# Optimization experiments

Hardware: AMD Instinct MI355X
Metric: run time of the kernel (lower is better)

The kernel has to match this reference:

```python
import jax, jax.numpy as jnp
import numpy as np

NEG_SLOPE = 0.2


def setup_inputs() -> dict:
    key = jax.random.key(0)
    k1, k2, k3 = jax.random.split(key, 3)
    bs, n_agents, input_dim = 32, 512, 128
    n_heads, hidden_dim = 8, 64
    h = jax.random.normal(k1, (bs, n_agents, input_dim), dtype=jnp.float32)
    # Linear(input_dim, n_heads*hidden_dim, bias=False), stored as [in, out]
    W = jax.random.normal(k2, (input_dim, n_heads * hidden_dim), dtype=jnp.float32) * (1.0 / np.sqrt(input_dim))
    # xavier_uniform with gain=1.414 on shape (1, n_heads, 2*hidden_dim)
    fan = n_heads + 2 * hidden_dim
    bound = 1.414 * np.sqrt(6.0 / fan)
    att_a = jax.random.uniform(k3, (1, n_heads, 2 * hidden_dim), dtype=jnp.float32,
                               minval=-bound, maxval=bound)
    return {"h": h, "W": W, "att_a": att_a}


def reference(h, W, att_a):
    bs, n_agents, _ = h.shape
    n_heads = att_a.shape[1]
    hidden_dim = att_a.shape[2] // 2
    # h_prime: [bs, n_heads, n_agents, hidden_dim]
    h_prime = (h @ W).reshape(bs, n_agents, n_heads, hidden_dim).transpose(0, 2, 1, 3)
    # Additive score decomposes exactly: (a1.h_i + a2.h_j) == sum(cat(h_i,h_j)*a)
    a_src = att_a[0, :, :hidden_dim]   # [n_heads, hidden_dim]
    a_dst = att_a[0, :, hidden_dim:]   # [n_heads, hidden_dim]
    e_src = jnp.einsum('bhnd,hd->bhn', h_prime, a_src)  # score contribution of node i (row)
    e_dst = jnp.einsum('bhnd,hd->bhn', h_prime, a_dst)  # contribution of node j (col)
    e = e_src[:, :, :, None] + e_dst[:, :, None, :]     # [bs, n_heads, n, n]
    e = jnp.where(e >= 0, e, NEG_SLOPE * e)             # leaky_relu(0.2)
    attention = jax.nn.softmax(e, axis=-1)
    h_new = jnp.einsum('bhnm,bhmd->bhnd', attention, h_prime)
    return jax.nn.elu(h_new)
```

## Files before the change

### kernel.cpp

```cpp
#include <hip/hip_runtime.h>

#define BS 32
#define NA 512
#define ID 128
#define NH 8
#define HD 64
#define NHD 512
#define NEG 0.2f
#define NC 32
#define CH 16
#define NW 8
#define BPAD 136

typedef short bf16x8 __attribute__((ext_vector_type(8)));
typedef float f32x4 __attribute__((ext_vector_type(4)));

__device__ inline unsigned f2bf_bits(float x) {
  unsigned u = __float_as_uint(x);
  return (u + 0x7FFFu + ((u >> 16) & 1u)) >> 16;
}

__device__ inline void split8(const float4& x, const float4& y,
                              bf16x8& hi, bf16x8& lo) {
  float f[8] = {x.x, x.y, x.z, x.w, y.x, y.y, y.z, y.w};
  #pragma unroll
  for (int j = 0; j < 8; ++j) {
    unsigned hb = f2bf_bits(f[j]);
    float r = f[j] - __uint_as_float(hb << 16);
    unsigned lb = f2bf_bits(r);
    hi[j] = (short)hb;
    lo[j] = (short)lb;
  }
}

__global__ __launch_bounds__(256, 4) void k1_mfma(
    const float* __restrict__ h, const float* __restrict__ W,
    float* __restrict__ io) {
  __shared__ unsigned short Bhi[64 * BPAD];
  __shared__ unsigned short Blo[64 * BPAD];

  int blk = blockIdx.x;
  int mt = blk >> 3;
  int n0 = (blk & 7) * 64;
  int m0 = mt * 128;
  int b = mt >> 2;
  int nbase = (mt & 3) * 128;
  int head = n0 >> 6;
  int t = threadIdx.x;
  int lane = t & 63, w = t >> 6;
  int q = lane >> 4, ml = lane & 15;

  {
    int c = t & 63, kq = t >> 6;
    const float* wsrc = W + (size_t)kq * 32 * NHD + n0 + c;
    #pragma unroll 4
    for (int kk = 0; kk < 32; ++kk) {
      int k = kq * 32 + kk;
      float x = wsrc[(size_t)kk * NHD];
      unsigned hb = f2bf_bits(x);
      float r = x - __uint_as_float(hb << 16);
      Bhi[c * BPAD + k] = (unsigned short)hb;
      Blo[c * BPAD + k] = (unsigned short)f2bf_bits(r);
    }
  }
  __syncthreads();

  f32x4 acc[2][4];
  #pragma unroll
  for (int mf = 0; mf < 2; ++mf)
    #pragma unroll
    for (int nf = 0; nf < 4; ++nf)
      acc[mf][nf] = (f32x4){0.f, 0.f, 0.f, 0.f};

  const float* A0 = h + (size_t)(m0 + w * 32 + ml) * ID;

  #pragma unroll
  for (int ks = 0; ks < 4; ++ks) {
    int ko = ks * 32 + q * 8;
    bf16x8 ah[2], al[2];
    #pragma unroll
    for (int mf = 0; mf < 2; ++mf) {
      const float* ap = A0 + mf * 16 * ID + ko;
      float4 f0 = *(const float4*)ap;
      float4 f1 = *(const float4*)(ap + 4);
      split8(f0, f1, ah[mf], al[mf]);
    }
    #pragma unroll
    for (int nf = 0; nf < 4; ++nf) {
      int bo = (nf * 16 + ml) * BPAD + ko;
      bf16x8 bh = *(const bf16x8*)&Bhi[bo];
      bf16x8 bl = *(const bf16x8*)&Blo[bo];
      #pragma unroll
      for (int mf = 0; mf < 2; ++mf) {
        acc[mf][nf] = __builtin_amdgcn_mfma_f32_16x16x32_bf16(ah[mf], bh, acc[mf][nf], 0, 0, 0);
        acc[mf][nf] = __builtin_amdgcn_mfma_f32_16x16x32_bf16(ah[mf], bl, acc[mf][nf], 0, 0, 0);
        acc[mf][nf] = __builtin_amdgcn_mfma_f32_16x16x32_bf16(al[mf], bh, acc[mf][nf], 0, 0, 0);
      }
    }
  }

  {
    float* ob = io + (((size_t)b * NH + head) * NA + nbase + w * 32) * HD + ml;
    #pragma unroll
    for (int mf = 0; mf < 2; ++mf)
      #pragma unroll
      for (int nf = 0; nf < 4; ++nf)
        #pragma unroll
        for (int r = 0; r < 4; ++r)
          ob[(size_t)(mf * 16 + q * 4 + r) * HD + nf * 16] = acc[mf][nf][r];
  }
}

__global__ __launch_bounds__(512, 2) void k2_fused(
    const float* __restrict__ att, float* __restrict__ io) {
  __shared__ float tv[NA]; __shared__ int tpm[NA];
  __shared__ float sv[NA]; __shared__ int spm[NA];
  __shared__ float wp[NA]; __shared__ float wn[NA];
  __shared__ float rawP8[NW * 64]; __shared__ float rawN8[NW * 64];
  __shared__ float sufPc[(NW + 1) * 64]; __shared__ float preNc[(NW + 1) * 64];
  __shared__ float zps[NA + 1]; __shared__ float znp[NA + 1];
  __shared__ float szP[NC]; __shared__ float szN[NC];
  __shared__ float sufZ[NC + 1]; __shared__ float preZ[NC + 1];
  __shared__ float4 abi[NA];
  __shared__ int jsr[NA];
  __shared__ int Earr[NA];
  __shared__ float asrc[HD]; __shared__ float adst[HD];

  int bh = blockIdx.x;
  int head = bh & (NH - 1);
  int t = threadIdx.x;
  int lane = t & 63, w = t >> 6;
  float* vbase = io + (size_t)bh * NA * HD;

  if (t < 2 * HD) {
    float a = att[head * 2 * HD + t];
    if (t < HD) asrc[t] = a; else adst[t - HD] = a;
  }
  __syncthreads();

  float vt, vs; int it = t, is_ = t;
  {
    const float4* vr = (const float4*)(vbase + (size_t)t * HD);
    float s0 = 0.f, s1 = 0.f, t0 = 0.f, t1 = 0.f;
    #pragma unroll
    for (int j = 0; j < HD / 4; j += 2) {
      float4 v0 = vr[j], v1 = vr[j + 1];
      s0 += v0.x*asrc[4*j+0] + v0.y*asrc[4*j+1] + v0.z*asrc[4*j+2] + v0.w*asrc[4*j+3];
      t0 += v0.x*adst[4*j+0] + v0.y*adst[4*j+1] + v0.z*adst[4*j+2] + v0.w*adst[4*j+3];
      s1 += v1.x*asrc[4*j+4] + v1.y*asrc[4*j+5] + v1.z*asrc[4*j+6] + v1.w*asrc[4*j+7];
      t1 += v1.x*adst[4*j+4] + v1.y*adst[4*j+5] + v1.z*adst[4*j+6] + v1.w*adst[4*j+7];
    }
    vs = s0 + s1; vt = t0 + t1;
  }

  for (int size = 2; size <= NA; size <<= 1) {
    bool dirAsc = ((t & size) == 0);
    for (int stride = size >> 1; stride > 0; stride >>= 1) {
      float pt, ps; int pit, pis;
      if (stride >= 64) {
        tv[t] = vt; tpm[t] = it; sv[t] = vs; spm[t] = is_;
        __syncthreads();
        pt = tv[t ^ stride]; pit = tpm[t ^ stride];
        ps = sv[t ^ stride]; pis = spm[t ^ stride];
        __syncthreads();
      } else {
        pt = __shfl_xor(vt, stride, 64); pit = __shfl_xor(it, stride, 64);
        ps = __shfl_xor(vs, stride, 64); pis = __shfl_xor(is_, stride, 64);
      }
      bool mn = (((t & stride) == 0) == dirAsc);
      if (mn ? (pt < vt) : (pt > vt)) { vt = pt; it = pit; }
      if (mn ? (ps < vs) : (ps > vs)) { vs = ps; is_ = pis; }
    }
  }
  tv[t] = vt; tpm[t] = it; sv[t] = vs; spm[t] = is_;
  __syncthreads();

  float cmax = fmaxf(tv[NA - 1], 0.f);
  float amax = fmaxf(sv[NA - 1], 0.f);
  wp[t] = __expf(vt - cmax);
  wn[t] = __expf(NEG * vt - cmax);
  __syncthreads();

  float vreg[64];
  {
    float aP = 0.f, aN = 0.f;
    #pragma unroll
    for (int jj = 0; jj < 64; ++jj) {
      int j = (w << 6) + jj;
      float vv = vbase[(size_t)tpm[j] * HD + lane];
      vreg[jj] = vv;
      aP += wp[j] * vv;
      aN += wn[j] * vv;
    }
    rawP8[(w << 6) + lane] = aP;
    rawN8[(w << 6) + lane] = aN;
  }
  __syncthreads();

  if (t < 64) {
    int d = t; float run = 0.f;
    sufPc[NW * 64 + d] = 0.f;
    for (int ww = NW - 1; ww >= 0; --ww) {
      run += rawP8[ww * 64 + d]; sufPc[ww * 64 + d] = run;
    }
  } else if (t < 128) {
    int d = t - 64; float run = 0.f;
    for (int ww = 0; ww <= NW; ++ww) {
      preNc[ww * 64 + d] = run;
      if (ww < NW) run += rawN8[ww * 64 + d];
    }
  } else if (t < 160) {
    int c = t - 128; float a = 0.f;
    for (int j = c * CH; j < c * CH + CH; ++j) a += wp[j];
    szP[c] = a;
  } else if (t < 192) {
    int c = t - 160; float a = 0.f;
    for (int j = c * CH; j < c * CH + CH; ++j) a += wn[j];
    szN[c] = a;
  }
  __syncthreads();

  if (t == 0) {
    float run = 0.f; sufZ[NC] = 0.f;
    for (int cc = NC - 1; cc >= 0; --cc) { run += szP[cc]; sufZ[cc] = run; }
  } else if (t == 1) {
    float run = 0.f;
    for (int cc = 0; cc <= NC; ++cc) { preZ[cc] = run; if (cc < NC) run += szN[cc]; }
  }
  __syncthreads();

  {
    int ch = t >> 4;
    float a = 0.f;
    for (int k = t; k < ch * CH + CH; ++k) a += wp[k];
    zps[t] = a + sufZ[ch + 1];
    float b2 = 0.f;
    for (int k = ch * CH; k < t; ++k) b2 += wn[k];
    znp[t] = preZ[ch] + b2;
    if (t == 0) { zps[NA] = 0.f; znp[NA] = preZ[NC]; }
  }
  __syncthreads();

  {
    float A = __expf(vs - amax);
    float B = __expf(NEG * vs - amax);
    float key = -vs;
    int lo = 0, hi = NA;
    while (lo < hi) { int mid = (lo + hi) >> 1; if (tv[mid] < key) lo = mid + 1; else hi = mid; }
    float den = A * zps[lo] + B * znp[lo];
    float4 qv; qv.x = A; qv.y = B; qv.z = 1.f / den; qv.w = __int_as_float(is_);
    abi[t] = qv;
    jsr[t] = lo;
  }
  __syncthreads();

  {
    int lo = 0, hi = NA;
    while (lo < hi) { int mid = (lo + hi) >> 1; if (jsr[mid] > t) lo = mid + 1; else hi = mid; }
    Earr[t] = lo;
  }
  __syncthreads();

  {
    float sufPv = sufPc[w * 64 + lane];
    float preSeedN = preNc[w * 64 + lane];
    float runN = 0.f;
    size_t obase = (size_t)bh * NA * HD + lane;
    int eprev = (w == 0) ? NA : Earr[(w << 6) - 1];
    #pragma unroll
    for (int jj = 0; jj < 64; ++jj) {
      int j = (w << 6) + jj;
      int ecur = Earr[j];
      float preNv = preSeedN + runN;
      for (int r = ecur; r < eprev; ++r) {
        float4 qv = abi[r];
        float x = (qv.x * sufPv + qv.y * preNv) * qv.z;
        int orow = __float_as_int(qv.w);
        io[obase + (size_t)orow * HD] = x > 0.f ? x : __expf(x) - 1.f;
      }
      float vv = vreg[jj];
      sufPv -= wp[j] * vv;
      runN  += wn[j] * vv;
      eprev = ecur;
    }
    if (w == NW - 1) {
      float preNv = preSeedN + runN;
      for (int r = 0; r < eprev; ++r) {
        float4 qv = abi[r];
        float x = (qv.y * preNv) * qv.z;
        int orow = __float_as_int(qv.w);
        io[obase + (size_t)orow * HD] = x > 0.f ? x : __expf(x) - 1.f;
      }
    }
  }
}

extern "C" void kernel_launch(void* const* d_in, const int* in_sizes, int n_in,
                              void* d_out, int out_size, void* d_ws, size_t ws_size,
                              hipStream_t stream) {
  const float* h   = (const float*)d_in[0];
  const float* W   = (const float*)d_in[1];
  const float* att = (const float*)d_in[2];
  float* io = (float*)d_out;
  (void)d_ws; (void)ws_size;

  k1_mfma <<<dim3(1024),    dim3(256), 0, stream>>>(h, W, io);
  k2_fused<<<dim3(BS * NH), dim3(512), 0, stream>>>(att, io);
}
```

Measured before the change: 126.1 us.

## Double attention-kernel block to 1024 threads and recompute per-row softmax factors inline

The fused attention kernel now runs with 1024 threads, or 16 waves, per block. Each wave sweeps 32 sorted columns instead of 64, and the sort and prefix-sum stages are guarded to the first 512 threads. The precomputed float4 per-row table (A, B, 1/den, row index) is removed. The output loop now recomputes the two exponentials and the reciprocal from the sorted scores and zps/znp, which saves shared memory and one barrier phase. This gives each CU more waves to hide global-store latency, at the cost of extra transcendental work per output element and idle threads in the sort phase.

After: 133.1 us. +5.5%, slower.

```diff
diff --git a/kernel.cpp b/kernel.cpp
--- a/kernel.cpp
+++ b/kernel.cpp
@@ -9,7 +9,7 @@
 #define NEG 0.2f
 #define NC 32
 #define CH 16
-#define NW 8
+#define NW2 16
 #define BPAD 136
 
 typedef short bf16x8 __attribute__((ext_vector_type(8)));
@@ -111,17 +111,15 @@
   }
 }
 
-__global__ __launch_bounds__(512, 2) void k2_fused(
+__global__ __launch_bounds__(1024) void k2_fused(
     const float* __restrict__ att, float* __restrict__ io) {
   __shared__ float tv[NA]; __shared__ int tpm[NA];
   __shared__ float sv[NA]; __shared__ int spm[NA];
   __shared__ float wp[NA]; __shared__ float wn[NA];
-  __shared__ float rawP8[NW * 64]; __shared__ float rawN8[NW * 64];
-  __shared__ float sufPc[(NW + 1) * 64]; __shared__ float preNc[(NW + 1) * 64];
+  __shared__ float sufPc[(NW2 + 1) * 64]; __shared__ float preNc[(NW2 + 1) * 64];
   __shared__ float zps[NA + 1]; __shared__ float znp[NA + 1];
   __shared__ float szP[NC]; __shared__ float szN[NC];
   __shared__ float sufZ[NC + 1]; __shared__ float preZ[NC + 1];
-  __shared__ float4 abi[NA];
   __shared__ int jsr[NA];
   __shared__ int Earr[NA];
   __shared__ float asrc[HD]; __shared__ float adst[HD];
@@ -138,8 +136,8 @@
   }
   __syncthreads();
 
-  float vt, vs; int it = t, is_ = t;
-  {
+  float vt = 0.f, vs = 0.f; int it = t, is_ = t;
+  if (t < NA) {
     const float4* vr = (const float4*)(vbase + (size_t)t * HD);
     float s0 = 0.f, s1 = 0.f, t0 = 0.f, t1 = 0.f;
     #pragma unroll
@@ -156,59 +154,72 @@
   for (int size = 2; size <= NA; size <<= 1) {
     bool dirAsc = ((t & size) == 0);
     for (int stride = size >> 1; stride > 0; stride >>= 1) {
-      float pt, ps; int pit, pis;
       if (stride >= 64) {
-        tv[t] = vt; tpm[t] = it; sv[t] = vs; spm[t] = is_;
+        if (t < NA) {
+          tv[t] = vt; tpm[t] = it; sv[t] = vs; spm[t] = is_;
+        }
         __syncthreads();
-        pt = tv[t ^ stride]; pit = tpm[t ^ stride];
-        ps = sv[t ^ stride]; pis = spm[t ^ stride];
+        if (t < NA) {
+          float pt = tv[t ^ stride]; int pit = tpm[t ^ stride];
+          float ps = sv[t ^ stride]; int pis = spm[t ^ stride];
+          bool mn = (((t & stride) == 0) == dirAsc);
+          if (mn ? (pt < vt) : (pt > vt)) { vt = pt; it = pit; }
+          if (mn ? (ps < vs) : (ps > vs)) { vs = ps; is_ = pis; }
+        }
         __syncthreads();
-      } else {
-        pt = __shfl_xor(vt, stride, 64); pit = __shfl_xor(it, stride, 64);
-        ps = __shfl_xor(vs, stride, 64); pis = __shfl_xor(is_, stride, 64);
+      } else if (t < NA) {
+        float pt = __shfl_xor(vt, stride, 64); int pit = __shfl_xor(it, stride, 64);
+        float ps = __shfl_xor(vs, stride, 64); int pis = __shfl_xor(is_, stride, 64);
+        bool mn = (((t & stride) == 0) == dirAsc);
+        if (mn ? (pt < vt) : (pt > vt)) { vt = pt; it = pit; }
+        if (mn ? (ps < vs) : (ps > vs)) { vs = ps; is_ = pis; }
       }
-      bool mn = (((t & stride) == 0) == dirAsc);
-      if (mn ? (pt < vt) : (pt > vt)) { vt = pt; it = pit; }
-      if (mn ? (ps < vs) : (ps > vs)) { vs = ps; is_ = pis; }
-    }
-  }
-  tv[t] = vt; tpm[t] = it; sv[t] = vs; spm[t] = is_;
+    }
+  }
+  if (t < NA) {
+    tv[t] = vt; tpm[t] = it; sv[t] = vs; spm[t] = is_;
+  }
   __syncthreads();
 
   float cmax = fmaxf(tv[NA - 1], 0.f);
   float amax = fmaxf(sv[NA - 1], 0.f);
-  wp[t] = __expf(vt - cmax);
-  wn[t] = __expf(NEG * vt - cmax);
-  __syncthreads();
-
-  float vreg[64];
+  if (t < NA) {
+    wp[t] = __expf(vt - cmax);
+    wn[t] = __expf(NEG * vt - cmax);
+  }
+  __syncthreads();
+
+  float vreg[32];
   {
     float aP = 0.f, aN = 0.f;
     #pragma unroll
-    for (int jj = 0; jj < 64; ++jj) {
-      int j = (w << 6) + jj;
+    for (int jj = 0; jj < 32; ++jj) {
+      int j = (w << 5) + jj;
       float vv = vbase[(size_t)tpm[j] * HD + lane];
       vreg[jj] = vv;
       aP += wp[j] * vv;
       aN += wn[j] * vv;
     }
-    rawP8[(w << 6) + lane] = aP;
-    rawN8[(w << 6) + lane] = aN;
+    sufPc[w * 64 + lane] = aP;
+    preNc[w * 64 + lane] = aN;
   }
   __syncthreads();
 
   if (t < 64) {
-    int d = t; float run = 0.f;
-    sufPc[NW * 64 + d] = 0.f;
-    for (int ww = NW - 1; ww >= 0; --ww) {
-      run += rawP8[ww * 64 + d]; sufPc[ww * 64 + d] = run;
+    float run = 0.f;
+    sufPc[NW2 * 64 + t] = 0.f;
+    for (int ww = NW2 - 1; ww >= 0; --ww) {
+      run += sufPc[ww * 64 + t];
+      sufPc[ww * 64 + t] = run;
     }
   } else if (t < 128) {
     int d = t - 64; float run = 0.f;
-    for (int ww = 0; ww <= NW; ++ww) {
+    for (int ww = 0; ww < NW2; ++ww) {
+      float raw = preNc[ww * 64 + d];
       preNc[ww * 64 + d] = run;
-      if (ww < NW) run += rawN8[ww * 64 + d];
-    }
+      run += raw;
+    }
+    preNc[NW2 * 64 + d] = run;
   } else if (t < 160) {
     int c = t - 128; float a = 0.f;
     for (int j = c * CH; j < c * CH + CH; ++j) a += wp[j];
@@ -229,7 +240,7 @@
   }
   __syncthreads();
 
-  {
+  if (t < NA) {
     int ch = t >> 4;
     float a = 0.f;
     for (int k = t; k < ch * CH + CH; ++k) a += wp[k];
@@ -238,23 +249,14 @@
     for (int k = ch * CH; k < t; ++k) b2 += wn[k];
     znp[t] = preZ[ch] + b2;
     if (t == 0) { zps[NA] = 0.f; znp[NA] = preZ[NC]; }
-  }
-  __syncthreads();
-
-  {
-    float A = __expf(vs - amax);
-    float B = __expf(NEG * vs - amax);
     float key = -vs;
     int lo = 0, hi = NA;
     while (lo < hi) { int mid = (lo + hi) >> 1; if (tv[mid] < key) lo = mid + 1; else hi = mid; }
-    float den = A * zps[lo] + B * znp[lo];
-    float4 qv; qv.x = A; qv.y = B; qv.z = 1.f / den; qv.w = __int_as_float(is_);
-    abi[t] = qv;
     jsr[t] = lo;
   }
   __syncthreads();
 
-  {
+  if (t < NA) {
     int lo = 0, hi = NA;
     while (lo < hi) { int mid = (lo + hi) >> 1; if (jsr[mid] > t) lo = mid + 1; else hi = mid; }
     Earr[t] = lo;
@@ -266,16 +268,19 @@
     float preSeedN = preNc[w * 64 + lane];
     float runN = 0.f;
     size_t obase = (size_t)bh * NA * HD + lane;
-    int eprev = (w == 0) ? NA : Earr[(w << 6) - 1];
-    #pragma unroll
-    for (int jj = 0; jj < 64; ++jj) {
-      int j = (w << 6) + jj;
+    int eprev = (w == 0) ? NA : Earr[(w << 5) - 1];
+    #pragma unroll 1
+    for (int jj = 0; jj < 32; ++jj) {
+      int j = (w << 5) + jj;
       int ecur = Earr[j];
       float preNv = preSeedN + runN;
       for (int r = ecur; r < eprev; ++r) {
-        float4 qv = abi[r];
-        float x = (qv.x * sufPv + qv.y * preNv) * qv.z;
-        int orow = __float_as_int(qv.w);
+        float s = sv[r];
+        float A = __expf(s - amax);
+        float B = __expf(NEG * s - amax);
+        float inv = 1.f / (A * zps[j] + B * znp[j]);
+        float x = (A * sufPv + B * preNv) * inv;
+        int orow = spm[r];
         io[obase + (size_t)orow * HD] = x > 0.f ? x : __expf(x) - 1.f;
       }
       float vv = vreg[jj];
@@ -283,12 +288,15 @@
       runN  += wn[j] * vv;
       eprev = ecur;
     }
-    if (w == NW - 1) {
+    if (w == NW2 - 1) {
       float preNv = preSeedN + runN;
       for (int r = 0; r < eprev; ++r) {
-        float4 qv = abi[r];
-        float x = (qv.y * preNv) * qv.z;
-        int orow = __float_as_int(qv.w);
+        float s = sv[r];
+        float A = __expf(s - amax);
+        float B = __expf(NEG * s - amax);
+        float inv = 1.f / (A * zps[NA] + B * znp[NA]);
+        float x = (B * preNv) * inv;
+        int orow = spm[r];
         io[obase + (size_t)orow * HD] = x > 0.f ? x : __expf(x) - 1.f;
       }
     }
@@ -304,6 +312,6 @@
   float* io = (float*)d_out;
   (void)d_ws; (void)ws_size;
 
-  k1_mfma <<<dim3(1024),    dim3(256), 0, stream>>>(h, W, io);
-  k2_fused<<<dim3(BS * NH), dim3(512), 0, stream>>>(att, io);
-}
+  k1_mfma <<<dim3(1024),    dim3(256),  0, stream>>>(h, W, io);
+  k2_fused<<<dim3(BS * NH), dim3(1024), 0, stream>>>(att, io);
+}
```

## Stage gathered value rows in LDS instead of registers and recompute per-row softmax terms

Applied to the files above, without the earlier changes.

Each gathered value row is now kept in a 128 KB shared-memory buffer instead of a 64-entry register array. The sweep loop stays rolled and reloads values from LDS. The per-row A/B/denominator float4 table is removed, so these terms are recomputed inside the emit loop from the sorted scores and the zps/znp prefix arrays. Index arrays shrink to 16-bit. The aim is to cut register pressure and free LDS for the staging buffer, but the large LDS footprint drops occupancy to one block per CU and adds redundant exp/div work per output.

Result: slower. 137.0 us (+8.6%).

```diff
diff --git a/kernel.cpp b/kernel.cpp
--- a/kernel.cpp
+++ b/kernel.cpp
@@ -111,19 +111,17 @@
   }
 }
 
-__global__ __launch_bounds__(512, 2) void k2_fused(
+__global__ __launch_bounds__(512) void k2_fused(
     const float* __restrict__ att, float* __restrict__ io) {
-  __shared__ float tv[NA]; __shared__ int tpm[NA];
-  __shared__ float sv[NA]; __shared__ int spm[NA];
+  __shared__ float VS[NA * 64];
+  __shared__ float tv[NA]; __shared__ float sv[NA];
+  __shared__ unsigned short tpm[NA]; __shared__ unsigned short spm[NA];
   __shared__ float wp[NA]; __shared__ float wn[NA];
-  __shared__ float rawP8[NW * 64]; __shared__ float rawN8[NW * 64];
   __shared__ float sufPc[(NW + 1) * 64]; __shared__ float preNc[(NW + 1) * 64];
   __shared__ float zps[NA + 1]; __shared__ float znp[NA + 1];
   __shared__ float szP[NC]; __shared__ float szN[NC];
   __shared__ float sufZ[NC + 1]; __shared__ float preZ[NC + 1];
-  __shared__ float4 abi[NA];
-  __shared__ int jsr[NA];
-  __shared__ int Earr[NA];
+  __shared__ unsigned short jsr[NA]; __shared__ unsigned short Earr[NA];
   __shared__ float asrc[HD]; __shared__ float adst[HD];
 
   int bh = blockIdx.x;
@@ -158,10 +156,11 @@
     for (int stride = size >> 1; stride > 0; stride >>= 1) {
       float pt, ps; int pit, pis;
       if (stride >= 64) {
-        tv[t] = vt; tpm[t] = it; sv[t] = vs; spm[t] = is_;
+        tv[t] = vt; tpm[t] = (unsigned short)it;
+        sv[t] = vs; spm[t] = (unsigned short)is_;
         __syncthreads();
-        pt = tv[t ^ stride]; pit = tpm[t ^ stride];
-        ps = sv[t ^ stride]; pis = spm[t ^ stride];
+        pt = tv[t ^ stride]; pit = (int)tpm[t ^ stride];
+        ps = sv[t ^ stride]; pis = (int)spm[t ^ stride];
         __syncthreads();
       } else {
         pt = __shfl_xor(vt, stride, 64); pit = __shfl_xor(it, stride, 64);
@@ -172,7 +171,8 @@
       if (mn ? (ps < vs) : (ps > vs)) { vs = ps; is_ = pis; }
     }
   }
-  tv[t] = vt; tpm[t] = it; sv[t] = vs; spm[t] = is_;
+  tv[t] = vt; tpm[t] = (unsigned short)it;
+  sv[t] = vs; spm[t] = (unsigned short)is_;
   __syncthreads();
 
   float cmax = fmaxf(tv[NA - 1], 0.f);
@@ -181,34 +181,36 @@
   wn[t] = __expf(NEG * vt - cmax);
   __syncthreads();
 
-  float vreg[64];
   {
     float aP = 0.f, aN = 0.f;
-    #pragma unroll
+    #pragma unroll 4
     for (int jj = 0; jj < 64; ++jj) {
       int j = (w << 6) + jj;
       float vv = vbase[(size_t)tpm[j] * HD + lane];
-      vreg[jj] = vv;
+      VS[j * 64 + lane] = vv;
       aP += wp[j] * vv;
       aN += wn[j] * vv;
     }
-    rawP8[(w << 6) + lane] = aP;
-    rawN8[(w << 6) + lane] = aN;
+    sufPc[w * 64 + lane] = aP;
+    preNc[w * 64 + lane] = aN;
   }
   __syncthreads();
 
   if (t < 64) {
-    int d = t; float run = 0.f;
-    sufPc[NW * 64 + d] = 0.f;
+    float run = 0.f;
+    sufPc[NW * 64 + t] = 0.f;
     for (int ww = NW - 1; ww >= 0; --ww) {
-      run += rawP8[ww * 64 + d]; sufPc[ww * 64 + d] = run;
+      run += sufPc[ww * 64 + t];
+      sufPc[ww * 64 + t] = run;
     }
   } else if (t < 128) {
     int d = t - 64; float run = 0.f;
-    for (int ww = 0; ww <= NW; ++ww) {
+    for (int ww = 0; ww < NW; ++ww) {
+      float raw = preNc[ww * 64 + d];
       preNc[ww * 64 + d] = run;
-      if (ww < NW) run += rawN8[ww * 64 + d];
-    }
+      run += raw;
+    }
+    preNc[NW * 64 + d] = run;
   } else if (t < 160) {
     int c = t - 128; float a = 0.f;
     for (int j = c * CH; j < c * CH + CH; ++j) a += wp[j];
@@ -238,26 +240,17 @@
     for (int k = ch * CH; k < t; ++k) b2 += wn[k];
     znp[t] = preZ[ch] + b2;
     if (t == 0) { zps[NA] = 0.f; znp[NA] = preZ[NC]; }
-  }
-  __syncthreads();
-
-  {
-    float A = __expf(vs - amax);
-    float B = __expf(NEG * vs - amax);
     float key = -vs;
     int lo = 0, hi = NA;
     while (lo < hi) { int mid = (lo + hi) >> 1; if (tv[mid] < key) lo = mid + 1; else hi = mid; }
-    float den = A * zps[lo] + B * znp[lo];
-    float4 qv; qv.x = A; qv.y = B; qv.z = 1.f / den; qv.w = __int_as_float(is_);
-    abi[t] = qv;
-    jsr[t] = lo;
+    jsr[t] = (unsigned short)lo;
   }
   __syncthreads();
 
   {
     int lo = 0, hi = NA;
-    while (lo < hi) { int mid = (lo + hi) >> 1; if (jsr[mid] > t) lo = mid + 1; else hi = mid; }
-    Earr[t] = lo;
+    while (lo < hi) { int mid = (lo + hi) >> 1; if ((int)jsr[mid] > t) lo = mid + 1; else hi = mid; }
+    Earr[t] = (unsigned short)lo;
   }
   __syncthreads();
 
@@ -266,19 +259,23 @@
     float preSeedN = preNc[w * 64 + lane];
     float runN = 0.f;
     size_t obase = (size_t)bh * NA * HD + lane;
-    int eprev = (w == 0) ? NA : Earr[(w << 6) - 1];
-    #pragma unroll
+    int jb = w << 6;
+    int eprev = (w == 0) ? NA : (int)Earr[jb - 1];
+    #pragma unroll 1
     for (int jj = 0; jj < 64; ++jj) {
-      int j = (w << 6) + jj;
-      int ecur = Earr[j];
+      int j = jb + jj;
+      float vv = VS[j * 64 + lane];
+      int ecur = (int)Earr[j];
       float preNv = preSeedN + runN;
       for (int r = ecur; r < eprev; ++r) {
-        float4 qv = abi[r];
-        float x = (qv.x * sufPv + qv.y * preNv) * qv.z;
-        int orow = __float_as_int(qv.w);
+        float s = sv[r];
+        float A = __expf(s - amax);
+        float B = __expf(NEG * s - amax);
+        float inv = 1.f / (A * zps[j] + B * znp[j]);
+        float x = (A * sufPv + B * preNv) * inv;
+        int orow = (int)spm[r];
         io[obase + (size_t)orow * HD] = x > 0.f ? x : __expf(x) - 1.f;
       }
-      float vv = vreg[jj];
       sufPv -= wp[j] * vv;
       runN  += wn[j] * vv;
       eprev = ecur;
@@ -286,9 +283,12 @@
     if (w == NW - 1) {
       float preNv = preSeedN + runN;
       for (int r = 0; r < eprev; ++r) {
-        float4 qv = abi[r];
-        float x = (qv.y * preNv) * qv.z;
-        int orow = __float_as_int(qv.w);
+        float s = sv[r];
+        float A = __expf(s - amax);
+        float B = __expf(NEG * s - amax);
+        float inv = 1.f / (A * zps[NA] + B * znp[NA]);
+        float x = (B * preNv) * inv;
+        int orow = (int)spm[r];
         io[obase + (size_t)orow * HD] = x > 0.f ? x : __expf(x) - 1.f;
       }
     }
```

## Fuse attention score projections into GEMM epilogue and split k2 over hidden halves

Applied to the files above, without the earlier changes.

The GEMM kernel now computes the per-node source and destination attention scores in its epilogue, using cross-lane shuffles over its accumulators, and writes them to workspace. The second kernel no longer re-reads h_prime rows to form these scores. The second kernel also launches twice as many blocks, each handling 32 of the 64 hidden dims. This doubles parallelism but duplicates the sort, prefix and search work per block and leaves half of each wave idle in the column phases.

Result: slower. 150.0 us (+18.9%).

```diff
diff --git a/kernel.cpp b/kernel.cpp
--- a/kernel.cpp
+++ b/kernel.cpp
@@ -35,7 +35,8 @@
 
 __global__ __launch_bounds__(256, 4) void k1_mfma(
     const float* __restrict__ h, const float* __restrict__ W,
-    float* __restrict__ io) {
+    const float* __restrict__ att, float* __restrict__ io,
+    float* __restrict__ sG, float* __restrict__ tG) {
   __shared__ unsigned short Bhi[64 * BPAD];
   __shared__ unsigned short Blo[64 * BPAD];
 
@@ -109,49 +110,63 @@
         for (int r = 0; r < 4; ++r)
           ob[(size_t)(mf * 16 + q * 4 + r) * HD + nf * 16] = acc[mf][nf][r];
   }
+
+  {
+    float a_s[4], a_d[4];
+    #pragma unroll
+    for (int nf = 0; nf < 4; ++nf) {
+      a_s[nf] = att[head * 128 + nf * 16 + ml];
+      a_d[nf] = att[head * 128 + 64 + nf * 16 + ml];
+    }
+    #pragma unroll
+    for (int mf = 0; mf < 2; ++mf) {
+      #pragma unroll
+      for (int r = 0; r < 4; ++r) {
+        float sp = 0.f, tp = 0.f;
+        #pragma unroll
+        for (int nf = 0; nf < 4; ++nf) {
+          float c = acc[mf][nf][r];
+          sp += c * a_s[nf]; tp += c * a_d[nf];
+        }
+        #pragma unroll
+        for (int m = 1; m < 16; m <<= 1) {
+          sp += __shfl_xor(sp, m, 64);
+          tp += __shfl_xor(tp, m, 64);
+        }
+        if (ml == 0) {
+          int row = nbase + w * 32 + mf * 16 + q * 4 + r;
+          size_t o = ((size_t)b * NH + head) * NA + row;
+          sG[o] = sp; tG[o] = tp;
+        }
+      }
+    }
+  }
 }
 
 __global__ __launch_bounds__(512, 2) void k2_fused(
-    const float* __restrict__ att, float* __restrict__ io) {
+    const float* __restrict__ sG, const float* __restrict__ tG,
+    float* __restrict__ io) {
   __shared__ float tv[NA]; __shared__ int tpm[NA];
   __shared__ float sv[NA]; __shared__ int spm[NA];
   __shared__ float wp[NA]; __shared__ float wn[NA];
-  __shared__ float rawP8[NW * 64]; __shared__ float rawN8[NW * 64];
-  __shared__ float sufPc[(NW + 1) * 64]; __shared__ float preNc[(NW + 1) * 64];
+  __shared__ float rawP8[NW * 32]; __shared__ float rawN8[NW * 32];
+  __shared__ float sufPc[(NW + 1) * 32]; __shared__ float preNc[(NW + 1) * 32];
   __shared__ float zps[NA + 1]; __shared__ float znp[NA + 1];
   __shared__ float szP[NC]; __shared__ float szN[NC];
   __shared__ float sufZ[NC + 1]; __shared__ float preZ[NC + 1];
   __shared__ float4 abi[NA];
   __shared__ int jsr[NA];
   __shared__ int Earr[NA];
-  __shared__ float asrc[HD]; __shared__ float adst[HD];
-
-  int bh = blockIdx.x;
-  int head = bh & (NH - 1);
+
+  int blk = blockIdx.x;
+  int bh = blk >> 1;
+  int dbase = (blk & 1) * 32;
   int t = threadIdx.x;
   int lane = t & 63, w = t >> 6;
   float* vbase = io + (size_t)bh * NA * HD;
 
-  if (t < 2 * HD) {
-    float a = att[head * 2 * HD + t];
-    if (t < HD) asrc[t] = a; else adst[t - HD] = a;
-  }
-  __syncthreads();
-
-  float vt, vs; int it = t, is_ = t;
-  {
-    const float4* vr = (const float4*)(vbase + (size_t)t * HD);
-    float s0 = 0.f, s1 = 0.f, t0 = 0.f, t1 = 0.f;
-    #pragma unroll
-    for (int j = 0; j < HD / 4; j += 2) {
-      float4 v0 = vr[j], v1 = vr[j + 1];
-      s0 += v0.x*asrc[4*j+0] + v0.y*asrc[4*j+1] + v0.z*asrc[4*j+2] + v0.w*asrc[4*j+3];
-      t0 += v0.x*adst[4*j+0] + v0.y*adst[4*j+1] + v0.z*adst[4*j+2] + v0.w*adst[4*j+3];
-      s1 += v1.x*asrc[4*j+4] + v1.y*asrc[4*j+5] + v1.z*asrc[4*j+6] + v1.w*asrc[4*j+7];
-      t1 += v1.x*adst[4*j+4] + v1.y*adst[4*j+5] + v1.z*adst[4*j+6] + v1.w*adst[4*j+7];
-    }
-    vs = s0 + s1; vt = t0 + t1;
-  }
+  float vt = tG[(size_t)bh * NA + t]; int it = t;
+  float vs = sG[(size_t)bh * NA + t]; int is_ = t;
 
   for (int size = 2; size <= NA; size <<= 1) {
     bool dirAsc = ((t & size) == 0);
@@ -182,39 +197,39 @@
   __syncthreads();
 
   float vreg[64];
-  {
+  if (lane < 32) {
     float aP = 0.f, aN = 0.f;
-    #pragma unroll
+    #pragma unroll 4
     for (int jj = 0; jj < 64; ++jj) {
       int j = (w << 6) + jj;
-      float vv = vbase[(size_t)tpm[j] * HD + lane];
+      float vv = vbase[(size_t)tpm[j] * HD + dbase + lane];
       vreg[jj] = vv;
       aP += wp[j] * vv;
       aN += wn[j] * vv;
     }
-    rawP8[(w << 6) + lane] = aP;
-    rawN8[(w << 6) + lane] = aN;
-  }
-  __syncthreads();
-
-  if (t < 64) {
+    rawP8[w * 32 + lane] = aP;
+    rawN8[w * 32 + lane] = aN;
+  }
+  __syncthreads();
+
+  if (t < 32) {
     int d = t; float run = 0.f;
-    sufPc[NW * 64 + d] = 0.f;
+    sufPc[NW * 32 + d] = 0.f;
     for (int ww = NW - 1; ww >= 0; --ww) {
-      run += rawP8[ww * 64 + d]; sufPc[ww * 64 + d] = run;
-    }
-  } else if (t < 128) {
-    int d = t - 64; float run = 0.f;
+      run += rawP8[ww * 32 + d]; sufPc[ww * 32 + d] = run;
+    }
+  } else if (t < 64) {
+    int d = t - 32; float run = 0.f;
     for (int ww = 0; ww <= NW; ++ww) {
-      preNc[ww * 64 + d] = run;
-      if (ww < NW) run += rawN8[ww * 64 + d];
-    }
-  } else if (t < 160) {
-    int c = t - 128; float a = 0.f;
+      preNc[ww * 32 + d] = run;
+      if (ww < NW) run += rawN8[ww * 32 + d];
+    }
+  } else if (t < 96) {
+    int c = t - 64; float a = 0.f;
     for (int j = c * CH; j < c * CH + CH; ++j) a += wp[j];
     szP[c] = a;
-  } else if (t < 192) {
-    int c = t - 160; float a = 0.f;
+  } else if (t < 128) {
+    int c = t - 96; float a = 0.f;
     for (int j = c * CH; j < c * CH + CH; ++j) a += wn[j];
     szN[c] = a;
   }
@@ -261,15 +276,16 @@
   }
   __syncthreads();
 
-  {
-    float sufPv = sufPc[w * 64 + lane];
-    float preSeedN = preNc[w * 64 + lane];
+  if (lane < 32) {
+    float sufPv = sufPc[w * 32 + lane];
+    float preSeedN = preNc[w * 32 + lane];
     float runN = 0.f;
-    size_t obase = (size_t)bh * NA * HD + lane;
-    int eprev = (w == 0) ? NA : Earr[(w << 6) - 1];
-    #pragma unroll
+    size_t obase = (size_t)bh * NA * HD + dbase + lane;
+    int jb = w << 6;
+    int eprev = (w == 0) ? NA : Earr[jb - 1];
+    #pragma unroll 1
     for (int jj = 0; jj < 64; ++jj) {
-      int j = (w << 6) + jj;
+      int j = jb + jj;
       int ecur = Earr[j];
       float preNv = preSeedN + runN;
       for (int r = ecur; r < eprev; ++r) {
@@ -302,8 +318,10 @@
   const float* W   = (const float*)d_in[1];
   const float* att = (const float*)d_in[2];
   float* io = (float*)d_out;
-  (void)d_ws; (void)ws_size;
-
-  k1_mfma <<<dim3(1024),    dim3(256), 0, stream>>>(h, W, io);
-  k2_fused<<<dim3(BS * NH), dim3(512), 0, stream>>>(att, io);
-}
+  const size_t R = (size_t)BS * NH * NA;
+  float* sG = (float*)d_ws;
+  float* tG = sG + R;
+
+  k1_mfma <<<dim3(1024),        dim3(256), 0, stream>>>(h, W, att, io, sG, tG);
+  k2_fused<<<dim3(BS * NH * 2), dim3(512), 0, stream>>>(sG, tG, io);
+}
```
